# Kernel optimization log

Measured on AMD Instinct MI355X. Metric: run time of the kernel, lower is better.

Reference implementation:

```python
import jax, jax.numpy as jnp
import numpy as np

B, S, D = 2, 1024, 1024
C, HID, H = 32, 64, 16  # compress_dim, prg_hidden_dim, num_heads


def setup_inputs() -> dict:
    key = jax.random.key(0)
    ks = jax.random.split(key, 7)
    def glorot(k, shape):
        lim = 1.0 / np.sqrt(shape[0])
        return jax.random.uniform(k, shape, jnp.float32, -lim, lim)
    return {
        "x": jax.random.normal(ks[0], (B, S, D), jnp.float32),
        "Wc": glorot(ks[1], (D, C)),
        "bc": jnp.zeros((C,), jnp.float32),
        "W1": glorot(ks[2], (2 * C, HID)),
        "b1": jnp.zeros((HID,), jnp.float32),
        "W2": glorot(ks[3], (HID, H)),
        "b2": jnp.zeros((H,), jnp.float32),
    }


def reference(x, Wc, bc, W1, b1, W2, b2):
    Bc, Sc, _ = x.shape
    # compress: [B,S,C]
    xc = x @ Wc + bc
    # pairwise concat via broadcast (same values as tile+concat)
    token_i = jnp.broadcast_to(xc[:, :, None, :], (Bc, Sc, Sc, C))
    token_j = jnp.broadcast_to(xc[:, None, :, :], (Bc, Sc, Sc, C))
    pair_emb = jnp.concatenate([token_i, token_j], axis=-1)  # [B,S,S,2C]
    h = jax.nn.gelu(pair_emb @ W1 + b1)                      # [B,S,S,HID]
    prg_bias = h @ W2 + b2                                   # [B,S,S,H]
    return jnp.transpose(prg_bias, (0, 3, 1, 2))             # [B,H,S,S]
```

## Files before the change

### kernel.cpp

```cpp
#include <hip/hip_runtime.h>
#include <hip/hip_fp16.h>

#define SDIM 1024

typedef _Float16 f16;
typedef _Float16 f16x2v __attribute__((ext_vector_type(2)));
typedef _Float16 f16x8 __attribute__((ext_vector_type(8)));
typedef __attribute__((ext_vector_type(4))) float f32x4;

union FragH { unsigned int u[4]; f16x8 f; };
union H2U  { unsigned int u; __half2 h; f16x2v v; };

__device__ __forceinline__ unsigned int addgelu_pair(unsigned int au, unsigned int bu) {
    const __half2 kC5  = __float2half2_rn(-0.006912f);
    const __half2 kC4  = __float2half2_rn( 0.019336f);
    const __half2 kC3  = __float2half2_rn(-0.040316f);
    const __half2 kC2  = __float2half2_rn( 0.090220f);
    const __half2 kC1  = __float2half2_rn(-0.185452f);
    const __half2 kC0  = __float2half2_rn( 0.455649f);
    const __half2 kXA  = __float2half2_rn( 0.2222222f);
    const __half2 kXB  = __float2half2_rn(-1.0f);
    const __half2 kHalf= __float2half2_rn( 0.5f);
    const f16x2v vHi = { (f16)3.0f, (f16)3.0f };
    const f16x2v vLo = { (f16)-3.0f, (f16)-3.0f };
    H2U A, B, T, C, G;
    A.u = au; B.u = bu;
    __half2 t  = __hadd2(A.h, B.h);
    T.h = t;
    C.v = __builtin_elementwise_min(__builtin_elementwise_max(T.v, vLo), vHi);
    __half2 tc = C.h;
    __half2 s  = __hmul2(tc, tc);
    __half2 x  = __hfma2(s, kXA, kXB);
    __half2 w  = __hfma2(kC5, x, kC4);
    w = __hfma2(w, x, kC3);
    w = __hfma2(w, x, kC2);
    w = __hfma2(w, x, kC1);
    w = __hfma2(w, x, kC0);
    __half2 m  = __hmul2(tc, w);
    __half2 sg = __hfma2(m, kHalf, kHalf);
    G.h = __hmul2(t, sg);
    return G.u;
}

__global__ __launch_bounds__(256) void compute_uv(
    const float* __restrict__ x, const float* __restrict__ Wc,
    const float* __restrict__ bc, const float* __restrict__ W1,
    const float* __restrict__ b1, f16* __restrict__ u, f16* __restrict__ v)
{
    __shared__ float xrow[4 * 1024];
    __shared__ float part[4 * 8 * 32];
    __shared__ float xc[4 * 32];
    const int tid = threadIdx.x;
    const size_t bs0 = (size_t)blockIdx.x * 4;

    const float4* xin = (const float4*)(x + bs0 * 1024);
    #pragma unroll
    for (int it = 0; it < 4; ++it)
        ((float4*)xrow)[it * 256 + tid] = xin[it * 256 + tid];
    __syncthreads();

    {
        const int c = tid & 31, p = tid >> 5;
        float acc[4] = {0.f, 0.f, 0.f, 0.f};
        #pragma unroll 4
        for (int dd = 0; dd < 128; ++dd) {
            const int d = p * 128 + dd;
            const float wv = Wc[d * 32 + c];
            #pragma unroll
            for (int r = 0; r < 4; ++r)
                acc[r] = __builtin_fmaf(xrow[r * 1024 + d], wv, acc[r]);
        }
        #pragma unroll
        for (int r = 0; r < 4; ++r)
            part[r * 256 + p * 32 + c] = acc[r];
    }
    __syncthreads();
    if (tid < 128) {
        const int r = tid >> 5, c = tid & 31;
        float s = bc[c];
        #pragma unroll
        for (int p = 0; p < 8; ++p) s += part[r * 256 + p * 32 + c];
        xc[r * 32 + c] = s;
    }
    __syncthreads();
    {
        const int h = tid & 63;
        const int rr = tid >> 6;
        float ua = b1[h], va = 0.0f;
        #pragma unroll
        for (int cc = 0; cc < 32; ++cc) {
            const float xv = xc[rr * 32 + cc];
            ua = __builtin_fmaf(xv, W1[cc * 64 + h], ua);
            va = __builtin_fmaf(xv, W1[(32 + cc) * 64 + h], va);
        }
        u[(bs0 + rr) * 64 + h] = (f16)ua;
        v[(bs0 + rr) * 64 + h] = (f16)va;
    }
}

__global__ __launch_bounds__(256) void prg_main(
    const f16* __restrict__ u, const f16* __restrict__ v,
    const float* __restrict__ W2, const float* __restrict__ b2,
    float* __restrict__ out)
{
    const int tid  = threadIdx.x;
    const int lane = tid & 63;
    const int w    = tid >> 6;
    const int jb   = blockIdx.x * 64;
    const int ib   = blockIdx.y * 16;
    const int b    = blockIdx.z;

    __shared__ f16 u_lds[16][64];

    if (tid < 128) {
        const int row = tid >> 3;
        const int col = (tid & 7) * 8;
        *(uint4*)&u_lds[row][col] =
            *(const uint4*)(u + ((size_t)(b * SDIM + ib + row) * 64 + col));
    }

    const int lg = lane >> 4;
    const int lr = lane & 15;
    const int k0 = lg * 8;

    const int jA = jb + w * 16 + lr;
    const f16* vp = v + ((size_t)(b * SDIM + jA) * 64);
    const uint4 vlo = *(const uint4*)(vp + k0);
    const uint4 vhi = *(const uint4*)(vp + k0 + 32);

    FragH w2lo, w2hi;
    #pragma unroll
    for (int e = 0; e < 4; ++e) {
        H2U a, c;
        a.h = __floats2half2_rn(W2[(k0 + 2*e) * 16 + lr],      W2[(k0 + 2*e + 1) * 16 + lr]);
        c.h = __floats2half2_rn(W2[(k0 + 32 + 2*e) * 16 + lr], W2[(k0 + 32 + 2*e + 1) * 16 + lr]);
        w2lo.u[e] = a.u;
        w2hi.u[e] = c.u;
    }

    const float b2h = b2[lr];

    __syncthreads();

    float* ob = out + ((size_t)(b * 16 + lr) * SDIM + ib) * SDIM + (jb + w * 16 + lg * 4);

    #pragma unroll 4
    for (int il = 0; il < 16; ++il) {
        const uint4 alo = *(const uint4*)&u_lds[il][k0];
        const uint4 ahi = *(const uint4*)&u_lds[il][k0 + 32];

        FragH glo, ghi;
        glo.u[0] = addgelu_pair(alo.x, vlo.x);
        glo.u[1] = addgelu_pair(alo.y, vlo.y);
        glo.u[2] = addgelu_pair(alo.z, vlo.z);
        glo.u[3] = addgelu_pair(alo.w, vlo.w);
        ghi.u[0] = addgelu_pair(ahi.x, vhi.x);
        ghi.u[1] = addgelu_pair(ahi.y, vhi.y);
        ghi.u[2] = addgelu_pair(ahi.z, vhi.z);
        ghi.u[3] = addgelu_pair(ahi.w, vhi.w);

        f32x4 acc = {b2h, b2h, b2h, b2h};
        acc = __builtin_amdgcn_mfma_f32_16x16x32_f16(glo.f, w2lo.f, acc, 0, 0, 0);
        acc = __builtin_amdgcn_mfma_f32_16x16x32_f16(ghi.f, w2hi.f, acc, 0, 0, 0);

        *(float4*)(ob + (size_t)il * SDIM) = *(float4*)&acc;
    }
}

extern "C" void kernel_launch(void* const* d_in, const int* in_sizes, int n_in,
                              void* d_out, int out_size, void* d_ws, size_t ws_size,
                              hipStream_t stream) {
    const float* x  = (const float*)d_in[0];
    const float* Wc = (const float*)d_in[1];
    const float* bc = (const float*)d_in[2];
    const float* W1 = (const float*)d_in[3];
    const float* b1 = (const float*)d_in[4];
    const float* W2 = (const float*)d_in[5];
    const float* b2 = (const float*)d_in[6];
    float* out = (float*)d_out;

    f16* u = (f16*)d_ws;
    f16* v = u + 2 * SDIM * 64;

    compute_uv<<<dim3(512), dim3(256), 0, stream>>>(x, Wc, bc, W1, b1, u, v);
    prg_main<<<dim3(16, 64, 2), dim3(256), 0, stream>>>(u, v, W2, b2, out);
}
```

Baseline: 49.67 us.

## Retile prg_main to 32x32 blocks, pre-convert W2 to fp16, batch stores

The first kernel now also writes a transposed fp16 copy of W2, so each prg_main thread loads its W2 fragment with two 16-byte loads instead of sixteen scalar loads plus conversions. prg_main switches from 64x16 tiles to 32x32 tiles with a 2x2 wave layout. It computes four rows of MFMA results before storing them, and sets launch_bounds(256,6) to raise occupancy. The intent is to cut per-block setup overhead and add memory-level parallelism on the output stores. The cost is higher register pressure and a slightly different store pattern, where each wave now writes 16-column segments across more rows.

```diff
diff --git a/kernel.cpp b/kernel.cpp
--- a/kernel.cpp
+++ b/kernel.cpp
@@ -8,7 +8,7 @@
 typedef _Float16 f16x8 __attribute__((ext_vector_type(8)));
 typedef __attribute__((ext_vector_type(4))) float f32x4;
 
-union FragH { unsigned int u[4]; f16x8 f; };
+union FragH { unsigned int u[4]; f16x8 f; uint4 q; };
 union H2U  { unsigned int u; __half2 h; f16x2v v; };
 
 __device__ __forceinline__ unsigned int addgelu_pair(unsigned int au, unsigned int bu) {
@@ -45,7 +45,8 @@
 __global__ __launch_bounds__(256) void compute_uv(
     const float* __restrict__ x, const float* __restrict__ Wc,
     const float* __restrict__ bc, const float* __restrict__ W1,
-    const float* __restrict__ b1, f16* __restrict__ u, f16* __restrict__ v)
+    const float* __restrict__ b1, const float* __restrict__ W2,
+    f16* __restrict__ u, f16* __restrict__ v, f16* __restrict__ W2h)
 {
     __shared__ float xrow[4 * 1024];
     __shared__ float part[4 * 8 * 32];
@@ -53,12 +54,20 @@
     const int tid = threadIdx.x;
     const size_t bs0 = (size_t)blockIdx.x * 4;
 
+    if (blockIdx.x == 0) {
+        #pragma unroll
+        for (int e = 0; e < 4; ++e) {
+            const int flat = tid * 4 + e;
+            const int h = flat >> 6, k = flat & 63;
+            W2h[flat] = (f16)W2[k * 16 + h];
+        }
+    }
+
     const float4* xin = (const float4*)(x + bs0 * 1024);
     #pragma unroll
     for (int it = 0; it < 4; ++it)
         ((float4*)xrow)[it * 256 + tid] = xin[it * 256 + tid];
     __syncthreads();
-
     {
         const int c = tid & 31, p = tid >> 5;
         float acc[4] = {0.f, 0.f, 0.f, 0.f};
@@ -98,21 +107,21 @@
     }
 }
 
-__global__ __launch_bounds__(256) void prg_main(
+__global__ __launch_bounds__(256, 6) void prg_main(
     const f16* __restrict__ u, const f16* __restrict__ v,
-    const float* __restrict__ W2, const float* __restrict__ b2,
+    const f16* __restrict__ W2h, const float* __restrict__ b2,
     float* __restrict__ out)
 {
     const int tid  = threadIdx.x;
     const int lane = tid & 63;
     const int w    = tid >> 6;
-    const int jb   = blockIdx.x * 64;
-    const int ib   = blockIdx.y * 16;
+    const int jb   = blockIdx.x * 32;
+    const int ib   = blockIdx.y * 32;
     const int b    = blockIdx.z;
 
-    __shared__ f16 u_lds[16][64];
+    __shared__ f16 u_lds[32][64];
 
-    if (tid < 128) {
+    {
         const int row = tid >> 3;
         const int col = (tid & 7) * 8;
         *(uint4*)&u_lds[row][col] =
@@ -122,48 +131,48 @@
     const int lg = lane >> 4;
     const int lr = lane & 15;
     const int k0 = lg * 8;
+    const int jw = jb + (w & 1) * 16;
+    const int iw = (w >> 1) * 16;
 
-    const int jA = jb + w * 16 + lr;
-    const f16* vp = v + ((size_t)(b * SDIM + jA) * 64);
+    const f16* vp = v + ((size_t)(b * SDIM + jw + lr) * 64);
     const uint4 vlo = *(const uint4*)(vp + k0);
     const uint4 vhi = *(const uint4*)(vp + k0 + 32);
 
     FragH w2lo, w2hi;
-    #pragma unroll
-    for (int e = 0; e < 4; ++e) {
-        H2U a, c;
-        a.h = __floats2half2_rn(W2[(k0 + 2*e) * 16 + lr],      W2[(k0 + 2*e + 1) * 16 + lr]);
-        c.h = __floats2half2_rn(W2[(k0 + 32 + 2*e) * 16 + lr], W2[(k0 + 32 + 2*e + 1) * 16 + lr]);
-        w2lo.u[e] = a.u;
-        w2hi.u[e] = c.u;
-    }
+    w2lo.q = *(const uint4*)(W2h + lr * 64 + k0);
+    w2hi.q = *(const uint4*)(W2h + lr * 64 + k0 + 32);
 
     const float b2h = b2[lr];
 
     __syncthreads();
 
-    float* ob = out + ((size_t)(b * 16 + lr) * SDIM + ib) * SDIM + (jb + w * 16 + lg * 4);
+    float* ob = out + ((size_t)(b * 16 + lr) * SDIM + (ib + iw)) * SDIM + jw + lg * 4;
 
-    #pragma unroll 4
-    for (int il = 0; il < 16; ++il) {
-        const uint4 alo = *(const uint4*)&u_lds[il][k0];
-        const uint4 ahi = *(const uint4*)&u_lds[il][k0 + 32];
-
-        FragH glo, ghi;
-        glo.u[0] = addgelu_pair(alo.x, vlo.x);
-        glo.u[1] = addgelu_pair(alo.y, vlo.y);
-        glo.u[2] = addgelu_pair(alo.z, vlo.z);
-        glo.u[3] = addgelu_pair(alo.w, vlo.w);
-        ghi.u[0] = addgelu_pair(ahi.x, vhi.x);
-        ghi.u[1] = addgelu_pair(ahi.y, vhi.y);
-        ghi.u[2] = addgelu_pair(ahi.z, vhi.z);
-        ghi.u[3] = addgelu_pair(ahi.w, vhi.w);
-
-        f32x4 acc = {b2h, b2h, b2h, b2h};
-        acc = __builtin_amdgcn_mfma_f32_16x16x32_f16(glo.f, w2lo.f, acc, 0, 0, 0);
-        acc = __builtin_amdgcn_mfma_f32_16x16x32_f16(ghi.f, w2hi.f, acc, 0, 0, 0);
-
-        *(float4*)(ob + (size_t)il * SDIM) = *(float4*)&acc;
+    #pragma unroll
+    for (int g = 0; g < 4; ++g) {
+        f32x4 acc[4];
+        #pragma unroll
+        for (int q = 0; q < 4; ++q) {
+            const int il = iw + g * 4 + q;
+            const uint4 alo = *(const uint4*)&u_lds[il][k0];
+            const uint4 ahi = *(const uint4*)&u_lds[il][k0 + 32];
+            FragH glo, ghi;
+            glo.u[0] = addgelu_pair(alo.x, vlo.x);
+            glo.u[1] = addgelu_pair(alo.y, vlo.y);
+            glo.u[2] = addgelu_pair(alo.z, vlo.z);
+            glo.u[3] = addgelu_pair(alo.w, vlo.w);
+            ghi.u[0] = addgelu_pair(ahi.x, vhi.x);
+            ghi.u[1] = addgelu_pair(ahi.y, vhi.y);
+            ghi.u[2] = addgelu_pair(ahi.z, vhi.z);
+            ghi.u[3] = addgelu_pair(ahi.w, vhi.w);
+            f32x4 a = {b2h, b2h, b2h, b2h};
+            a = __builtin_amdgcn_mfma_f32_16x16x32_f16(glo.f, w2lo.f, a, 0, 0, 0);
+            a = __builtin_amdgcn_mfma_f32_16x16x32_f16(ghi.f, w2hi.f, a, 0, 0, 0);
+            acc[q] = a;
+        }
+        #pragma unroll
+        for (int q = 0; q < 4; ++q)
+            *(float4*)(ob + (size_t)(g * 4 + q) * SDIM) = *(float4*)&acc[q];
     }
 }
 
@@ -179,9 +188,10 @@
     const float* b2 = (const float*)d_in[6];
     float* out = (float*)d_out;
 
-    f16* u = (f16*)d_ws;
-    f16* v = u + 2 * SDIM * 64;
+    f16* u   = (f16*)d_ws;
+    f16* v   = u + 2 * SDIM * 64;
+    f16* W2h = v + 2 * SDIM * 64;
 
-    compute_uv<<<dim3(512), dim3(256), 0, stream>>>(x, Wc, bc, W1, b1, u, v);
-    prg_main<<<dim3(16, 64, 2), dim3(256), 0, stream>>>(u, v, W2, b2, out);
+    compute_uv<<<dim3(512), dim3(256), 0, stream>>>(x, Wc, bc, W1, b1, W2, u, v, W2h);
+    prg_main<<<dim3(32, 32, 2), dim3(256), 0, stream>>>(u, v, W2h, b2, out);
 }
```

Measured after the change: 49.76 us. Within noise of the previous version (+0.2%).
